# Performance work log

Measured on AMD Instinct MI355X. Metric: run time of the kernel, lower is better.

The kernel has to match this reference:

```python
import jax, jax.numpy as jnp
import numpy as np

B, T, D, H, DK, DV = 2, 2048, 1024, 16, 64, 64
_MASK_ADDER = -10000.0  # tf-models MaskedSoftmax convention


def setup_inputs() -> dict:
    key = jax.random.key(0)
    ks = jax.random.split(key, 8)
    s = 0.02
    return {
        "query": jax.random.normal(ks[0], (B, T, D), jnp.float32),
        "value": jax.random.normal(ks[1], (B, T, D), jnp.float32),
        "Wq": jax.random.normal(ks[2], (D, H, DK), jnp.float32) * s,
        "bq": jnp.zeros((H, DK), jnp.float32),
        "Wk": jax.random.normal(ks[3], (D, H, DK), jnp.float32) * s,
        "bk": jnp.zeros((H, DK), jnp.float32),
        "Wv": jax.random.normal(ks[4], (D, H, DV), jnp.float32) * s,
        "bv": jnp.zeros((H, DV), jnp.float32),
        "Wo": jax.random.normal(ks[5], (H, DV, D), jnp.float32) * s,
        "bo": jnp.zeros((D,), jnp.float32),
        "attention_mask": jnp.ones((B, T, T), jnp.int32),
    }


def reference(query, value, Wq, bq, Wk, bk, Wv, bv, Wo, bo, attention_mask):
    # key defaults to value (call() with key=None); training=False -> no dropout
    q = jnp.einsum("btd,dhk->bthk", query, Wq) + bq          # [B,T,H,DK]
    k = jnp.einsum("bsd,dhk->bshk", value, Wk) + bk          # [B,S,H,DK]
    v = jnp.einsum("bsd,dhk->bshk", value, Wv) + bv          # [B,S,H,DV]
    q = q * (1.0 / jnp.sqrt(jnp.asarray(DK, q.dtype)))
    scores = jnp.einsum("bthk,bshk->bhts", q, k)             # [B,H,T,S]
    # MaskedSoftmax: expand mask at axis 1, additive -10000 on masked slots
    adder = (1.0 - attention_mask.astype(scores.dtype))[:, None, :, :] * _MASK_ADDER
    probs = jax.nn.softmax(scores + adder, axis=-1)
    ctx = jnp.einsum("bhts,bshv->bthv", probs, v)            # [B,T,H,DV]
    out = jnp.einsum("bthv,hvd->btd", ctx, Wo) + bo          # [B,T,D]
    return out
```

## Files before the change

kernel.cpp:

```cpp
#include <hip/hip_runtime.h>
#include <hip/hip_bf16.h>
#include <stdint.h>

#define TSEQ 2048
#define DMODEL 1024
#define NHEAD 16
#define HDIM 64
#define MROWS 4096
#define L2E 1.44269504088896340736f

typedef unsigned short u16;
typedef unsigned int u32;
typedef __attribute__((ext_vector_type(8))) short bf16x8;
typedef __attribute__((ext_vector_type(8))) unsigned short u16x8;
typedef __attribute__((ext_vector_type(4))) unsigned short u16x4;
typedef __attribute__((ext_vector_type(4))) float f32x4;
typedef __attribute__((ext_vector_type(16))) float f32x16;
typedef __attribute__((ext_vector_type(4))) unsigned int u32x4;

__device__ inline u16 f2bf(float f) {
  __hip_bfloat16 h(f);
  return __builtin_bit_cast(u16, h);
}

__device__ inline float fexp2(float x) { float r; asm("v_exp_f32 %0, %1" : "=v"(r) : "v"(x)); return r; }

__device__ inline unsigned cvtpk_bf16(float a, float b) {
  unsigned r; asm("v_cvt_pk_bf16_f32 %0, %1, %2" : "=v"(r) : "v"(a), "v"(b)); return r;
}

__device__ inline float fmax3(float a, float b, float c) {
  float r; asm("v_max3_f32 %0, %1, %2, %3" : "=v"(r) : "v"(a), "v"(b), "v"(c)); return r;
}

__device__ inline void permswap(u32& a, u32& b) {
  asm volatile("v_permlane32_swap_b32 %0, %1" : "+v"(a), "+v"(b));
}

__device__ inline void gload16(const void* g, void* l) {
  __builtin_amdgcn_global_load_lds((const __attribute__((address_space(1))) void*)g,
                                   (__attribute__((address_space(3))) void*)l, 16, 0, 0);
}

__global__ void prep(const float* __restrict__ q, const float* __restrict__ v,
                     u16* __restrict__ qo, u16* __restrict__ vo,
                     const float* __restrict__ Wq, const float* __restrict__ Wk,
                     const float* __restrict__ Wv, const float* __restrict__ Wo,
                     u16* __restrict__ WT3, u16* __restrict__ WoT,
                     const int* __restrict__ mask, int* __restrict__ flags) {
  __shared__ float tile[32][33];
  __shared__ int sred[4];
  const int bid = blockIdx.x, tid = threadIdx.x;
  if (bid < 8192) {
    const float* in = bid < 4096 ? q : v;
    u16* out = bid < 4096 ? qo : vo;
    const int i = (bid & 4095) * 1024 + tid * 4;
    float4 x = *(const float4*)(in + i);
    u16x4 o;
    o.x = f2bf(x.x); o.y = f2bf(x.y); o.z = f2bf(x.z); o.w = f2bf(x.w);
    *(u16x4*)(out + i) = o;
  } else if (bid < 12288) {
    int t = bid - 8192;
    const int z = t >> 10; t &= 1023;
    const float* W = z == 0 ? Wq : z == 1 ? Wk : z == 2 ? Wv : Wo;
    u16* WT = z < 3 ? (WT3 + (size_t)z * 1024 * 1024) : WoT;
    const int bx = t & 31, by = t >> 5;
    const int tr = tid >> 3;
    const int tc4 = (tid & 7) * 4;
    float4 x = *(const float4*)(W + (size_t)(by * 32 + tr) * 1024 + bx * 32 + tc4);
    tile[tr][tc4 + 0] = x.x; tile[tr][tc4 + 1] = x.y;
    tile[tr][tc4 + 2] = x.z; tile[tr][tc4 + 3] = x.w;
    __syncthreads();
    u16x4 o;
    o.x = f2bf(tile[tc4 + 0][tr]); o.y = f2bf(tile[tc4 + 1][tr]);
    o.z = f2bf(tile[tc4 + 2][tr]); o.w = f2bf(tile[tc4 + 3][tr]);
    *(u16x4*)(WT + (size_t)(bx * 32 + tr) * 1024 + by * 32 + tc4) = o;
  } else {
    const int t = bid - 12288;
    const int st = t & 15, qt = (t >> 4) & 15, b = t >> 8;
    const int row = qt * 128 + (tid >> 1);
    const int col0 = st * 128 + (tid & 1) * 64;
    const int* p = mask + (size_t)b * TSEQ * TSEQ + (size_t)row * TSEQ + col0;
    int ok = 1;
    #pragma unroll
    for (int j = 0; j < 64; j += 4) {
      int4 x = *(const int4*)(p + j);
      ok &= (x.x == 1) & (x.y == 1) & (x.z == 1) & (x.w == 1);
    }
    ok = __all(ok);
    if ((tid & 63) == 0) sred[tid >> 6] = ok;
    __syncthreads();
    if (tid == 0) flags[(b * 16 + qt) * 16 + st] = sred[0] & sred[1] & sred[2] & sred[3];
  }
}

__global__ __launch_bounds__(256) void gemm_qkv(
    const u16* __restrict__ qxb, const u16* __restrict__ vxb, const u16* __restrict__ WT3,
    const float* __restrict__ bq, const float* __restrict__ bk, const float* __restrict__ bv,
    u16* __restrict__ Qb, u16* __restrict__ Kb, u16* __restrict__ VTb, float qscale) {
  __shared__ u16 SMEM[2 * 128 * 64];
  u16* As = SMEM;
  u16* Bs = SMEM + 128 * 64;
  const int tid = threadIdx.x;
  const int w = tid >> 6, lane = tid & 63;
  const int lo = lane & 15, hi = lane >> 4;
  const int bid = blockIdx.x + (blockIdx.y << 5);
  const int swz = (bid & 7) * 96 + (bid >> 3);
  const int m0 = (swz & 31) << 7, n0 = (swz >> 5) << 7;
  const int nsel = n0 >> 10;
  const u16* A = nsel == 0 ? qxb : vxb;
  const float* bias = nsel == 0 ? bq : nsel == 1 ? bk : bv;
  const float scl = nsel == 0 ? qscale : 1.0f;
  const int wm = (w >> 1) * 64, wn = (w & 1) * 64;
  f32x4 acc[4][4] = {};
  const int loff = w * 4096 + lane * 16;
  for (int kt = 0; kt < 16; ++kt) {
    #pragma unroll
    for (int i = 0; i < 4; ++i) {
      const int off = loff + i * 1024;
      const int row = off >> 7;
      const int g = ((off >> 4) & 7) ^ (row & 7);
      gload16(A + (size_t)(m0 + row) * 1024 + kt * 64 + g * 8, (char*)As + off);
      gload16(WT3 + (size_t)(n0 + row) * 1024 + kt * 64 + g * 8, (char*)Bs + off);
    }
    __syncthreads();
    #pragma unroll
    for (int kk = 0; kk < 2; ++kk) {
      bf16x8 af[4], bfr[4];
      #pragma unroll
      for (int mi = 0; mi < 4; ++mi) {
        int row = wm + mi * 16 + lo;
        af[mi] = *(const bf16x8*)(As + row * 64 + (((kk * 4 + hi) ^ (row & 7)) << 3));
      }
      #pragma unroll
      for (int ni = 0; ni < 4; ++ni) {
        int row = wn + ni * 16 + lo;
        bfr[ni] = *(const bf16x8*)(Bs + row * 64 + (((kk * 4 + hi) ^ (row & 7)) << 3));
      }
      #pragma unroll
      for (int mi = 0; mi < 4; ++mi)
        #pragma unroll
        for (int ni = 0; ni < 4; ++ni)
          acc[mi][ni] = __builtin_amdgcn_mfma_f32_16x16x32_bf16(af[mi], bfr[ni], acc[mi][ni], 0, 0, 0);
    }
    __syncthreads();
  }
  if (nsel < 2) {
    u16* dst = nsel == 0 ? Qb : Kb;
    #pragma unroll
    for (int ni = 0; ni < 4; ++ni) {
      const int col = (n0 + wn + ni * 16 + lo) & 1023;
      const float bc = bias[col];
      #pragma unroll
      for (int mi = 0; mi < 4; ++mi) {
        #pragma unroll
        for (int r = 0; r < 4; ++r) {
          const int row = m0 + wm + mi * 16 + hi * 4 + r;
          const float v = (acc[mi][ni][r] + bc) * scl;
          dst[(size_t)(((row >> 11) * NHEAD + (col >> 6)) * TSEQ + (row & 2047)) * HDIM + (col & 63)] = f2bf(v);
        }
      }
    }
  } else {
    u16* T = SMEM;
    #pragma unroll
    for (int ni = 0; ni < 4; ++ni) {
      const int nl = wn + ni * 16 + lo;
      const float bc = bias[(n0 + nl) & 1023];
      #pragma unroll
      for (int mi = 0; mi < 4; ++mi) {
        const int mloc = wm + mi * 16 + hi * 4;
        u16x4 pk;
        #pragma unroll
        for (int r = 0; r < 4; ++r) pk[r] = f2bf(acc[mi][ni][r] + bc);
        const int cg = mloc >> 3, sub = mloc & 7;
        *(u16x4*)(T + nl * 128 + (((cg ^ (nl & 15)) << 3) + sub)) = pk;
      }
    }
    __syncthreads();
    const int b_ = m0 >> 11, t0_ = m0 & 2047;
    #pragma unroll
    for (int p = 0; p < 8; ++p) {
      const int nl = p * 16 + (tid >> 4);
      const int cg = tid & 15;
      u16x8 val = *(const u16x8*)(T + nl * 128 + ((cg ^ (nl & 15)) << 3));
      const int colg = (n0 + nl) & 1023;
      u16* dst = VTb + ((size_t)(b_ * NHEAD + (colg >> 6)) * 64 + (colg & 63)) * TSEQ + t0_ + cg * 8;
      *(u16x8*)dst = val;
    }
  }
}

__global__ __launch_bounds__(256) void gemm_o(const u16* __restrict__ A, const u16* __restrict__ BT,
                                              const float* __restrict__ bias, float* __restrict__ C) {
  __shared__ u16 As[64 * 64];
  __shared__ u16 Bs[128 * 64];
  const int tid = threadIdx.x;
  const int w = tid >> 6, lane = tid & 63;
  const int lo = lane & 15, hi = lane >> 4;
  const int bid = blockIdx.x + (blockIdx.y << 6);
  const int swz = (bid & 7) * 64 + (bid >> 3);
  const int m0 = (swz & 63) << 6, n0 = (swz >> 6) << 7;
  const int wm = (w >> 1) * 32, wn = (w & 1) * 64;
  f32x4 acc[2][4] = {};
  for (int kt = 0; kt < 16; ++kt) {
    #pragma unroll
    for (int i = 0; i < 2; ++i) {
      const int off = tid * 16 + i * 4096;
      const int row = off >> 7;
      const int g = ((off >> 4) & 7) ^ (row & 7);
      gload16(A + (size_t)(m0 + row) * 1024 + kt * 64 + g * 8, (char*)As + off);
    }
    #pragma unroll
    for (int i = 0; i < 4; ++i) {
      const int off = tid * 16 + i * 4096;
      const int row = off >> 7;
      const int g = ((off >> 4) & 7) ^ (row & 7);
      gload16(BT + (size_t)(n0 + row) * 1024 + kt * 64 + g * 8, (char*)Bs + off);
    }
    __syncthreads();
    #pragma unroll
    for (int kk = 0; kk < 2; ++kk) {
      bf16x8 af[2], bfr[4];
      #pragma unroll
      for (int mi = 0; mi < 2; ++mi) {
        int row = wm + mi * 16 + lo;
        af[mi] = *(const bf16x8*)(As + row * 64 + (((kk * 4 + hi) ^ (row & 7)) << 3));
      }
      #pragma unroll
      for (int ni = 0; ni < 4; ++ni) {
        int row = wn + ni * 16 + lo;
        bfr[ni] = *(const bf16x8*)(Bs + row * 64 + (((kk * 4 + hi) ^ (row & 7)) << 3));
      }
      #pragma unroll
      for (int mi = 0; mi < 2; ++mi)
        #pragma unroll
        for (int ni = 0; ni < 4; ++ni)
          acc[mi][ni] = __builtin_amdgcn_mfma_f32_16x16x32_bf16(af[mi], bfr[ni], acc[mi][ni], 0, 0, 0);
    }
    __syncthreads();
  }
  #pragma unroll
  for (int ni = 0; ni < 4; ++ni) {
    const int col = n0 + wn + ni * 16 + lo;
    const float bc = bias[col];
    #pragma unroll
    for (int mi = 0; mi < 2; ++mi)
      #pragma unroll
      for (int r = 0; r < 4; ++r) {
        const int row = m0 + wm + mi * 16 + hi * 4 + r;
        C[(size_t)row * DMODEL + col] = acc[mi][ni][r] + bc;
      }
  }
}

__global__ __launch_bounds__(256) void flash(
    const u16* __restrict__ Q, const u16* __restrict__ K, const u16* __restrict__ VT,
    const int* __restrict__ mask, const int* __restrict__ flags, u16* __restrict__ ctx) {
  __shared__ u16 Ks[2][64 * 64];
  __shared__ u16 Vs[3][64 * 64];
  const int tid = threadIdx.x, w = tid >> 6, lane = tid & 63;
  const int l5 = lane & 31, hi2 = lane >> 5;
  const int bid0 = blockIdx.x + (blockIdx.y << 4);
  const int swz = (bid0 & 7) * 64 + (bid0 >> 3);
  const int qt = swz & 15, bh = swz >> 4;
  const int b = bh >> 4, h = bh & 15;
  const int tq = qt * 128 + w * 32;

  const int soff = w * 2048 + lane * 16;
  const int srow0 = w * 16 + (lane >> 3);
  const int lg0 = (((lane & 7) ^ (lane >> 3) ^ ((w * 2) & 3)) << 3);
  const int lg1 = (((lane & 7) ^ (lane >> 3) ^ ((w * 2 + 1) & 3)) << 3);

  bf16x8 qf[4];
  #pragma unroll
  for (int kc = 0; kc < 4; ++kc)
    qf[kc] = *(const bf16x8*)(Q + ((size_t)bh * TSEQ + tq + l5) * 64 + kc * 16 + hi2 * 8);

  bf16x8 onesf;
  #pragma unroll
  for (int j = 0; j < 8; ++j) onesf[j] = (short)0x3F80;

  unsigned fl = 0;
  {
    const int* fp = flags + (b * 16 + qt) * 16;
    #pragma unroll
    for (int i = 0; i < 4; ++i) {
      int4 v = *(const int4*)(fp + i * 4);
      fl |= (unsigned)((v.x & 1) | ((v.y & 1) << 1) | ((v.z & 1) << 2) | ((v.w & 1) << 3)) << (4 * i);
    }
  }

  f32x16 o0 = {}, o1 = {}, o2 = {};
  float mrow = -1e30f;
  bf16x8 paA[4], paB[4];

#define STAGE_K(buf, st_) do {                                                        \
    const u16* kb_ = K + ((size_t)bh * TSEQ + (st_) * 64) * 64;                       \
    gload16(kb_ + (size_t)srow0 * 64 + lg0, (char*)Ks[buf] + soff);                   \
    gload16(kb_ + (size_t)(srow0 + 8) * 64 + lg1, (char*)Ks[buf] + soff + 1024);      \
  } while (0)
#define STAGE_V(buf, st_) do {                                                        \
    const u16* vb_ = VT + (size_t)bh * 64 * TSEQ + (st_) * 64;                        \
    gload16(vb_ + (size_t)srow0 * TSEQ + lg0, (char*)Vs[buf] + soff);                 \
    gload16(vb_ + (size_t)(srow0 + 8) * TSEQ + lg1, (char*)Vs[buf] + soff + 1024);    \
  } while (0)

#define FR(base, row, sg) \
  (*(const bf16x8*)((base) + (row) * 64 + ((((sg) ^ ((row) & 7) ^ (((row) >> 3) & 3)) << 3))))

#define QKC(T, S0, S1) do {                                                           \
    const u16* Kb_ = Ks[(T) & 1];                                                     \
    _Pragma("unroll") for (int kc = 0; kc < 4; ++kc) {                                \
      const int sg = kc * 2 + hi2;                                                    \
      S0 = __builtin_amdgcn_mfma_f32_32x32x16_bf16(FR(Kb_, l5, sg), qf[kc], S0, 0, 0, 0); \
      S1 = __builtin_amdgcn_mfma_f32_32x32x16_bf16(FR(Kb_, 32 + l5, sg), qf[kc], S1, 0, 0, 0); \
    } } while (0)

#define PVC(VB, PA) do {                                                              \
    const u16* Vb_ = Vs[VB];                                                          \
    _Pragma("unroll") for (int kc = 0; kc < 4; ++kc) {                                \
      const int sg = kc * 2 + hi2;                                                    \
      o0 = __builtin_amdgcn_mfma_f32_32x32x16_bf16(PA[kc], FR(Vb_, l5, sg), o0, 0, 0, 0); \
      o1 = __builtin_amdgcn_mfma_f32_32x32x16_bf16(PA[kc], FR(Vb_, 32 + l5, sg), o1, 0, 0, 0); \
      o2 = __builtin_amdgcn_mfma_f32_32x32x16_bf16(PA[kc], onesf, o2, 0, 0, 0);       \
    } } while (0)

#define SMAX(T, S0, S1, PAOUT) do {                                                   \
    if (!((fl >> ((T) >> 1)) & 1)) {                                                  \
      const int t_ = tq + l5;                                                         \
      const int* mp_ = mask + ((size_t)b * TSEQ + t_) * TSEQ + (T) * 64;              \
      _Pragma("unroll") for (int r = 0; r < 16; ++r) {                                \
        const int sr_ = (r & 3) + 8 * (r >> 2) + 4 * hi2;                             \
        S0[r] += (1.0f - (float)mp_[sr_]) * -14426.950408f;                           \
        S1[r] += (1.0f - (float)mp_[sr_ + 32]) * -14426.950408f;                      \
      } }                                                                             \
    float c0 = fmaxf(S0[0], S1[0]), c1 = fmaxf(S0[1], S1[1]);                         \
    float c2 = fmaxf(S0[2], S1[2]), c3 = fmaxf(S0[3], S1[3]);                         \
    _Pragma("unroll") for (int r = 4; r < 16; r += 4) {                               \
      c0 = fmax3(c0, S0[r], S1[r]);     c1 = fmax3(c1, S0[r+1], S1[r+1]);             \
      c2 = fmax3(c2, S0[r+2], S1[r+2]); c3 = fmax3(c3, S0[r+3], S1[r+3]); }           \
    float pm = fmax3(fmaxf(c0, c1), c2, c3);                                          \
    pm = fmaxf(pm, __shfl_xor(pm, 32));                                               \
    if (__any(pm - mrow > 11.0f)) {                                                   \
      const float mn_ = fmaxf(mrow, pm);                                              \
      const float a_ = fexp2(mrow - mn_);                                             \
      mrow = mn_;                                                                     \
      _Pragma("unroll") for (int r = 0; r < 16; ++r) {                                \
        const float ar_ = __shfl(a_, (r & 3) + 8 * (r >> 2) + 4 * hi2);               \
        o0[r] *= ar_; o1[r] *= ar_; o2[r] *= ar_; } }                                 \
    u32 W0_[8], W1_[8];                                                               \
    _Pragma("unroll") for (int q_ = 0; q_ < 4; ++q_)                                  \
      _Pragma("unroll") for (int c_ = 0; c_ < 2; ++c_) {                              \
        const int r = 4 * q_ + 2 * c_;                                                \
        float a0 = fexp2(S0[r] - mrow), b0 = fexp2(S0[r + 1] - mrow);                 \
        float a1 = fexp2(S1[r] - mrow), b1 = fexp2(S1[r + 1] - mrow);                 \
        W0_[q_ * 2 + c_] = cvtpk_bf16(a0, b0);                                        \
        W1_[q_ * 2 + c_] = cvtpk_bf16(a1, b1); }                                      \
    _Pragma("unroll") for (int ts = 0; ts < 2; ++ts)                                  \
      _Pragma("unroll") for (int qp = 0; qp < 2; ++qp) {                              \
        u32 d0 = ts ? W1_[(2 * qp) * 2 + 0] : W0_[(2 * qp) * 2 + 0];                  \
        u32 e0 = ts ? W1_[(2 * qp + 1) * 2 + 0] : W0_[(2 * qp + 1) * 2 + 0];          \
        u32 d1 = ts ? W1_[(2 * qp) * 2 + 1] : W0_[(2 * qp) * 2 + 1];                  \
        u32 e1 = ts ? W1_[(2 * qp + 1) * 2 + 1] : W0_[(2 * qp + 1) * 2 + 1];          \
        permswap(d0, e0); permswap(d1, e1);                                           \
        u32x4 fw_; fw_.x = d0; fw_.y = d1; fw_.z = e0; fw_.w = e1;                    \
        PAOUT[ts * 2 + qp] = __builtin_bit_cast(bf16x8, fw_); }                       \
  } while (0)

#define BODY(T, VPREV, VNEXT, DOSTAGE, PAIN, PAOUT) do {                              \
    if (DOSTAGE) { STAGE_K(((T) + 1) & 1, (T) + 1); STAGE_V(VNEXT, (T) + 1); }        \
    f32x16 s0 = {}, s1 = {};                                                          \
    __builtin_amdgcn_s_setprio(1);                                                    \
    QKC(T, s0, s1);                                                                   \
    PVC(VPREV, PAIN);                                                                 \
    __builtin_amdgcn_s_setprio(0);                                                    \
    SMAX(T, s0, s1, PAOUT);                                                           \
    __syncthreads();                                                                  \
  } while (0)

  STAGE_K(0, 0); STAGE_V(0, 0);
  __syncthreads();
  {
    f32x16 s0 = {}, s1 = {};
    __builtin_amdgcn_s_setprio(1);
    QKC(0, s0, s1);
    __builtin_amdgcn_s_setprio(0);
    STAGE_K(1, 1); STAGE_V(1, 1);
    SMAX(0, s0, s1, paA);
    __syncthreads();
  }

  int vp = 0, vn = 2;
  for (int t = 1; t < 31; t += 2) {
    BODY(t, vp, vn, 1, paA, paB);
    const int vp2 = (vp + 1 == 3) ? 0 : vp + 1;
    const int vn2 = (vn + 1 == 3) ? 0 : vn + 1;
    BODY(t + 1, vp2, vn2, 1, paB, paA);
    vp = (vp2 + 1 == 3) ? 0 : vp2 + 1;
    vn = (vn2 + 1 == 3) ? 0 : vn2 + 1;
  }
  BODY(31, vp, 0, 0, paA, paB);

  __builtin_amdgcn_s_setprio(1);
  PVC(1, paB);
  __builtin_amdgcn_s_setprio(0);

#undef BODY
#undef SMAX
#undef PVC
#undef QKC
#undef FR
#undef STAGE_V
#undef STAGE_K

  #pragma unroll
  for (int r = 0; r < 16; ++r) {
    const int sr = (r & 3) + 8 * (r >> 2) + 4 * hi2;
    const float ir = 1.0f / o2[r];
    u16* cp = ctx + (size_t)(b * TSEQ + tq + sr) * DMODEL + h * 64;
    cp[l5] = f2bf(o0[r] * ir);
    cp[32 + l5] = f2bf(o1[r] * ir);
  }
}

extern "C" void kernel_launch(void* const* d_in, const int* in_sizes, int n_in,
                              void* d_out, int out_size, void* d_ws, size_t ws_size,
                              hipStream_t stream) {
  (void)in_sizes; (void)n_in; (void)out_size; (void)ws_size;
  const float* query = (const float*)d_in[0];
  const float* value = (const float*)d_in[1];
  const float* Wq = (const float*)d_in[2];
  const float* bq = (const float*)d_in[3];
  const float* Wk = (const float*)d_in[4];
  const float* bk = (const float*)d_in[5];
  const float* Wv = (const float*)d_in[6];
  const float* bv = (const float*)d_in[7];
  const float* Wo = (const float*)d_in[8];
  const float* bo = (const float*)d_in[9];
  const int* amask = (const int*)d_in[10];

  char* ws = (char*)d_ws;
  const size_t MB = 1 << 20;
  u16* qxb = (u16*)(ws + 0 * MB);
  u16* vxb = (u16*)(ws + 8 * MB);
  u16* WT3 = (u16*)(ws + 16 * MB);
  u16* Qb  = (u16*)(ws + 24 * MB);
  u16* Kb  = (u16*)(ws + 32 * MB);
  int* flg = (int*)(ws + 42 * MB);
  u16* WoT = (u16*)(ws + 44 * MB);
  u16* VTb = (u16*)(ws + 48 * MB);
  u16* ctx = (u16*)(ws + 56 * MB);

  prep<<<12800, 256, 0, stream>>>(query, value, qxb, vxb, Wq, Wk, Wv, Wo, WT3, WoT, amask, flg);
  gemm_qkv<<<dim3(32, 24), 256, 0, stream>>>(qxb, vxb, WT3, bq, bk, bv, Qb, Kb, VTb, 0.125f * L2E);
  flash<<<dim3(16, 32), 256, 0, stream>>>(Qb, Kb, VTb, amask, flg, ctx);
  gemm_o<<<dim3(64, 8), 256, 0, stream>>>(ctx, WoT, bo, (float*)d_out);
}
```

Before: 142.9 us.

## Load K fragments directly into registers and compute row sums in VALU

K tiles now go straight from global memory into register fragments, double-buffered across iterations, instead of being staged through shared memory. The row-sum MFMA against a ones vector is replaced by a scalar running sum of the exponentials, combined across lane halves with a shuffle. This removes the K LDS traffic, a third of the PV MFMAs, and the o2 accumulator. In exchange it uses more registers (two 8-fragment K buffers), makes uncoalesced per-lane global loads, and sums fp32 probabilities rather than the bf16-rounded values actually fed to PV.

```diff
diff --git a/kernel.cpp b/kernel.cpp
--- a/kernel.cpp
+++ b/kernel.cpp
@@ -257,7 +257,6 @@
 __global__ __launch_bounds__(256) void flash(
     const u16* __restrict__ Q, const u16* __restrict__ K, const u16* __restrict__ VT,
     const int* __restrict__ mask, const int* __restrict__ flags, u16* __restrict__ ctx) {
-  __shared__ u16 Ks[2][64 * 64];
   __shared__ u16 Vs[3][64 * 64];
   const int tid = threadIdx.x, w = tid >> 6, lane = tid & 63;
   const int l5 = lane & 31, hi2 = lane >> 5;
@@ -277,10 +276,6 @@
   for (int kc = 0; kc < 4; ++kc)
     qf[kc] = *(const bf16x8*)(Q + ((size_t)bh * TSEQ + tq + l5) * 64 + kc * 16 + hi2 * 8);
 
-  bf16x8 onesf;
-  #pragma unroll
-  for (int j = 0; j < 8; ++j) onesf[j] = (short)0x3F80;
-
   unsigned fl = 0;
   {
     const int* fp = flags + (b * 16 + qt) * 16;
@@ -291,15 +286,20 @@
     }
   }
 
-  f32x16 o0 = {}, o1 = {}, o2 = {};
-  float mrow = -1e30f;
+  const u16* Kbh = K + (size_t)bh * TSEQ * 64;
+
+  f32x16 o0 = {}, o1 = {};
+  float mrow = -1e30f, lrow = 0.f;
   bf16x8 paA[4], paB[4];
-
-#define STAGE_K(buf, st_) do {                                                        \
-    const u16* kb_ = K + ((size_t)bh * TSEQ + (st_) * 64) * 64;                       \
-    gload16(kb_ + (size_t)srow0 * 64 + lg0, (char*)Ks[buf] + soff);                   \
-    gload16(kb_ + (size_t)(srow0 + 8) * 64 + lg1, (char*)Ks[buf] + soff + 1024);      \
-  } while (0)
+  bf16x8 kfA[8], kfB[8];
+
+#define KLOAD(KF, st_) do {                                                           \
+    const u16* kb_ = Kbh + (size_t)(st_) * 64 * 64;                                   \
+    _Pragma("unroll") for (int kc = 0; kc < 4; ++kc) {                                \
+      KF[kc * 2 + 0] = *(const bf16x8*)(kb_ + (size_t)l5 * 64 + (kc * 2 + hi2) * 8);  \
+      KF[kc * 2 + 1] = *(const bf16x8*)(kb_ + (size_t)(32 + l5) * 64 + (kc * 2 + hi2) * 8); \
+    } } while (0)
+
 #define STAGE_V(buf, st_) do {                                                        \
     const u16* vb_ = VT + (size_t)bh * 64 * TSEQ + (st_) * 64;                        \
     gload16(vb_ + (size_t)srow0 * TSEQ + lg0, (char*)Vs[buf] + soff);                 \
@@ -309,12 +309,10 @@
 #define FR(base, row, sg) \
   (*(const bf16x8*)((base) + (row) * 64 + ((((sg) ^ ((row) & 7) ^ (((row) >> 3) & 3)) << 3))))
 
-#define QKC(T, S0, S1) do {                                                           \
-    const u16* Kb_ = Ks[(T) & 1];                                                     \
+#define QKC(KF, S0, S1) do {                                                          \
     _Pragma("unroll") for (int kc = 0; kc < 4; ++kc) {                                \
-      const int sg = kc * 2 + hi2;                                                    \
-      S0 = __builtin_amdgcn_mfma_f32_32x32x16_bf16(FR(Kb_, l5, sg), qf[kc], S0, 0, 0, 0); \
-      S1 = __builtin_amdgcn_mfma_f32_32x32x16_bf16(FR(Kb_, 32 + l5, sg), qf[kc], S1, 0, 0, 0); \
+      S0 = __builtin_amdgcn_mfma_f32_32x32x16_bf16(KF[kc * 2 + 0], qf[kc], S0, 0, 0, 0); \
+      S1 = __builtin_amdgcn_mfma_f32_32x32x16_bf16(KF[kc * 2 + 1], qf[kc], S1, 0, 0, 0); \
     } } while (0)
 
 #define PVC(VB, PA) do {                                                              \
@@ -323,7 +321,6 @@
       const int sg = kc * 2 + hi2;                                                    \
       o0 = __builtin_amdgcn_mfma_f32_32x32x16_bf16(PA[kc], FR(Vb_, l5, sg), o0, 0, 0, 0); \
       o1 = __builtin_amdgcn_mfma_f32_32x32x16_bf16(PA[kc], FR(Vb_, 32 + l5, sg), o1, 0, 0, 0); \
-      o2 = __builtin_amdgcn_mfma_f32_32x32x16_bf16(PA[kc], onesf, o2, 0, 0, 0);       \
     } } while (0)
 
 #define SMAX(T, S0, S1, PAOUT) do {                                                   \
@@ -345,18 +342,20 @@
     if (__any(pm - mrow > 11.0f)) {                                                   \
       const float mn_ = fmaxf(mrow, pm);                                              \
       const float a_ = fexp2(mrow - mn_);                                             \
-      mrow = mn_;                                                                     \
+      lrow *= a_; mrow = mn_;                                                         \
       _Pragma("unroll") for (int r = 0; r < 16; ++r) {                                \
         const float ar_ = __shfl(a_, (r & 3) + 8 * (r >> 2) + 4 * hi2);               \
-        o0[r] *= ar_; o1[r] *= ar_; o2[r] *= ar_; } }                                 \
-    u32 W0_[8], W1_[8];                                                               \
+        o0[r] *= ar_; o1[r] *= ar_; } }                                               \
+    float rs = 0.f; u32 W0_[8], W1_[8];                                               \
     _Pragma("unroll") for (int q_ = 0; q_ < 4; ++q_)                                  \
       _Pragma("unroll") for (int c_ = 0; c_ < 2; ++c_) {                              \
         const int r = 4 * q_ + 2 * c_;                                                \
         float a0 = fexp2(S0[r] - mrow), b0 = fexp2(S0[r + 1] - mrow);                 \
         float a1 = fexp2(S1[r] - mrow), b1 = fexp2(S1[r + 1] - mrow);                 \
+        rs += (a0 + b0) + (a1 + b1);                                                  \
         W0_[q_ * 2 + c_] = cvtpk_bf16(a0, b0);                                        \
         W1_[q_ * 2 + c_] = cvtpk_bf16(a1, b1); }                                      \
+    rs += __shfl_xor(rs, 32); lrow += rs;                                             \
     _Pragma("unroll") for (int ts = 0; ts < 2; ++ts)                                  \
       _Pragma("unroll") for (int qp = 0; qp < 2; ++qp) {                              \
         u32 d0 = ts ? W1_[(2 * qp) * 2 + 0] : W0_[(2 * qp) * 2 + 0];                  \
@@ -368,39 +367,41 @@
         PAOUT[ts * 2 + qp] = __builtin_bit_cast(bf16x8, fw_); }                       \
   } while (0)
 
-#define BODY(T, VPREV, VNEXT, DOSTAGE, PAIN, PAOUT) do {                              \
-    if (DOSTAGE) { STAGE_K(((T) + 1) & 1, (T) + 1); STAGE_V(VNEXT, (T) + 1); }        \
+#define BODY(T, VPREV, VNEXT, DOSTAGE, PAIN, PAOUT, KIN, KOUT) do {                   \
+    if (DOSTAGE) { STAGE_V(VNEXT, (T) + 1); KLOAD(KOUT, (T) + 1); }                   \
     f32x16 s0 = {}, s1 = {};                                                          \
     __builtin_amdgcn_s_setprio(1);                                                    \
-    QKC(T, s0, s1);                                                                   \
+    QKC(KIN, s0, s1);                                                                 \
     PVC(VPREV, PAIN);                                                                 \
     __builtin_amdgcn_s_setprio(0);                                                    \
     SMAX(T, s0, s1, PAOUT);                                                           \
     __syncthreads();                                                                  \
   } while (0)
 
-  STAGE_K(0, 0); STAGE_V(0, 0);
+  KLOAD(kfA, 0);
+  STAGE_V(0, 0);
   __syncthreads();
   {
     f32x16 s0 = {}, s1 = {};
     __builtin_amdgcn_s_setprio(1);
-    QKC(0, s0, s1);
+    QKC(kfA, s0, s1);
     __builtin_amdgcn_s_setprio(0);
-    STAGE_K(1, 1); STAGE_V(1, 1);
+    KLOAD(kfB, 1);
+    STAGE_V(1, 1);
     SMAX(0, s0, s1, paA);
     __syncthreads();
   }
 
   int vp = 0, vn = 2;
   for (int t = 1; t < 31; t += 2) {
-    BODY(t, vp, vn, 1, paA, paB);
+    BODY(t, vp, vn, 1, paA, paB, kfB, kfA);
     const int vp2 = (vp + 1 == 3) ? 0 : vp + 1;
     const int vn2 = (vn + 1 == 3) ? 0 : vn + 1;
-    BODY(t + 1, vp2, vn2, 1, paB, paA);
+    BODY(t + 1, vp2, vn2, 1, paB, paA, kfA, kfB);
     vp = (vp2 + 1 == 3) ? 0 : vp2 + 1;
     vn = (vn2 + 1 == 3) ? 0 : vn2 + 1;
   }
-  BODY(31, vp, 0, 0, paA, paB);
+  BODY(31, vp, 0, 0, paA, paB, kfB, kfA);
 
   __builtin_amdgcn_s_setprio(1);
   PVC(1, paB);
@@ -412,12 +413,13 @@
 #undef QKC
 #undef FR
 #undef STAGE_V
-#undef STAGE_K
-
+#undef KLOAD
+
+  const float inv = 1.0f / lrow;
   #pragma unroll
   for (int r = 0; r < 16; ++r) {
     const int sr = (r & 3) + 8 * (r >> 2) + 4 * hi2;
-    const float ir = 1.0f / o2[r];
+    const float ir = __shfl(inv, sr);
     u16* cp = ctx + (size_t)(b * TSEQ + tq + sr) * DMODEL + h * 64;
     cp[l5] = f2bf(o0[r] * ir);
     cp[32 + l5] = f2bf(o1[r] * ir);
```

After: 156.5 us. +9.6%, slower.
